# Performance work log

Measured on AMD Instinct MI355X. Metric: run time of the kernel, lower is better.

Reference implementation:

```python
import jax, jax.numpy as jnp
import numpy as np

SEQ, BATCH, HIDDEN = 4096, 16, 512


def setup_inputs() -> dict:
    key = jax.random.key(0)
    ks = jax.random.split(key, 8)
    scale = 1.0 / np.sqrt(HIDDEN)
    outputs_hidden = jax.random.normal(ks[0], (1, BATCH, HIDDEN), jnp.float32)
    encoder_out = jax.random.normal(ks[1], (SEQ, BATCH, HIDDEN), jnp.float32)
    encoder_features = jax.random.normal(ks[2], (SEQ, BATCH, HIDDEN), jnp.float32)
    # binary-ish float mask, mostly ones
    encoder_mask = (jax.random.uniform(ks[3], (BATCH, 1, SEQ)) > 0.1).astype(jnp.float32)
    # running sum of positive exp-scores; keep strictly positive
    temporal_scores_sum = jax.random.uniform(ks[4], (BATCH, 1, SEQ)) + 0.5
    W_feat = jax.random.normal(ks[5], (HIDDEN, HIDDEN), jnp.float32) * scale
    b_feat = jax.random.normal(ks[6], (HIDDEN,), jnp.float32)
    v_attn = jax.random.normal(ks[7], (HIDDEN,), jnp.float32) * scale
    return {
        "outputs_hidden": outputs_hidden,
        "encoder_out": encoder_out,
        "encoder_features": encoder_features,
        "encoder_mask": encoder_mask,
        "temporal_scores_sum": temporal_scores_sum,
        "W_feat": W_feat,
        "b_feat": b_feat,
        "v_attn": v_attn,
    }


def reference(outputs_hidden, encoder_out, encoder_features, encoder_mask,
              temporal_scores_sum, W_feat, b_feat, v_attn):
    # self.features: Linear(hidden, hidden) on decoder state [1, b, h]
    decoder_features = jnp.einsum('obh,kh->obk', outputs_hidden, W_feat) + b_feat
    # additive score: tanh(dec + enc) . v  -> [s, b]
    scores = jnp.einsum('sbh,h->sb', jnp.tanh(decoder_features + encoder_features), v_attn)
    # Permute(1,2,0) of [s,b,1] -> [b,1,s], then exp
    temporal_attention = jnp.exp(scores).T[:, None, :]  # [b, 1, s]
    attention = temporal_attention / temporal_scores_sum
    new_scores_sum = temporal_attention + temporal_scores_sum
    attention = attention * encoder_mask
    attention = attention / jnp.sum(attention, axis=-1, keepdims=True)  # Normalize(-1)
    enc = jnp.transpose(encoder_out, (1, 0, 2))           # [b, s, h]
    context = jnp.matmul(attention, enc)                  # [b, 1, h]
    context = jnp.transpose(context, (1, 0, 2))           # [1, b, h]
    return context, attention, new_scores_sum
```

## Files before the change

kernel.cpp:

```cpp
#include <hip/hip_runtime.h>
#include <hip/hip_bf16.h>
#include <stdint.h>

#define SEQ 4096
#define BATCH 16
#define HID 512
#define ATT_OFF (BATCH * HID)
#define NSS_OFF (BATCH * HID + BATCH * SEQ)

#define SPW 4
#define NT 4
#define SBLK (4 * NT * SPW)
#define NGRP (SEQ / SBLK)
#define NSTREAM_BLOCKS (BATCH * NGRP)

typedef unsigned short u16;
typedef unsigned int u32;

__device__ __forceinline__ float bflo(u32 w) { return __uint_as_float(w << 16); }
__device__ __forceinline__ float bfhi(u32 w) { return __uint_as_float(w & 0xffff0000u); }

__device__ __forceinline__ u16 f2bf(float f) {
  u32 u = __float_as_uint(f);
  return (u16)((u + 0x7fffu + ((u >> 16) & 1u)) >> 16);
}

__device__ __forceinline__ int probe_bf16(const void* tssp) {
  const u16* t = (const u16*)tssp;
  int ok = 1;
  #pragma unroll
  for (int i = 0; i < 8; i += 2) {
    u16 u = t[i];
    ok &= (u >= 0x3F00 && u <= 0x3FC0) ? 1 : 0;
  }
  return ok;
}

template <int BF>
__device__ __forceinline__ float ld1(const void* p, size_t i) {
  if (BF) return __uint_as_float(((u32)((const u16*)p)[i]) << 16);
  return ((const float*)p)[i];
}

template <int BF>
__device__ __forceinline__ void st1(void* p, size_t i, float v) {
  if (BF) ((u16*)p)[i] = f2bf(v);
  else    ((float*)p)[i] = v;
}

template <int BF>
__device__ __forceinline__ void load8(const void* p, size_t e, float* o) {
  if (BF) {
    uint4 v = *(const uint4*)((const u16*)p + e);
    o[0]=bflo(v.x); o[1]=bfhi(v.x); o[2]=bflo(v.y); o[3]=bfhi(v.y);
    o[4]=bflo(v.z); o[5]=bfhi(v.z); o[6]=bflo(v.w); o[7]=bfhi(v.w);
  } else {
    const float4* f = (const float4*)((const float*)p + e);
    float4 a = f[0], b = f[1];
    o[0]=a.x; o[1]=a.y; o[2]=a.z; o[3]=a.w;
    o[4]=b.x; o[5]=b.y; o[6]=b.z; o[7]=b.w;
  }
}

__device__ __forceinline__ float fast_tanh(float x) {
  float e = __expf(2.0f * x);
  return 1.0f - 2.0f * __builtin_amdgcn_rcpf(e + 1.0f);
}

template <int BF>
__device__ __forceinline__ void k_dec_body(
    const void* oh, const void* W, const void* bias, float* dec) {
  int tid = threadIdx.x;
  int gw = blockIdx.x * 4 + (tid >> 6);
  int lane = tid & 63;
  int k = gw & (HID - 1);
  int b = gw >> 9;
  float wv[8], ov[8];
  load8<BF>(W,  (size_t)k * HID + lane * 8, wv);
  load8<BF>(oh, (size_t)b * HID + lane * 8, ov);
  float acc = 0.0f;
  #pragma unroll
  for (int j = 0; j < 8; ++j) acc += wv[j] * ov[j];
  #pragma unroll
  for (int off = 32; off; off >>= 1) acc += __shfl_xor(acc, off, 64);
  if (lane == 0) dec[b * HID + k] = acc + ld1<BF>(bias, k);
}

__global__ __launch_bounds__(256) void k_dec(
    const void* oh, const void* W, const void* bias, const void* tss,
    float* dec, float* denom) {
  if (blockIdx.x == 0 && threadIdx.x < BATCH) denom[threadIdx.x] = 0.0f;
  if (probe_bf16(tss)) k_dec_body<1>(oh, W, bias, dec);
  else                 k_dec_body<0>(oh, W, bias, dec);
}

template <int BF>
__device__ __forceinline__ void k_scores_body(
    const void* ef, const void* maskp, const void* tssp, const void* vp,
    const float* dec, float* w_buf, float* denom, void* out) {
  int tid = threadIdx.x, lane = tid & 63, wave = tid >> 6;
  int blk = blockIdx.x;
  int b = blk & (BATCH - 1);
  int grp = blk >> 4;
  int sw = grp * SBLK + wave * (NT * SPW);

  float dv[8], vv[8];
  #pragma unroll
  for (int j = 0; j < 8; ++j) dv[j] = dec[b * HID + lane * 8 + j];
  load8<BF>(vp, lane * 8, vv);

  float evA[SPW][8], evB[SPW][8];
  float tsA[SPW], tsB[SPW], mA[SPW], mB[SPW];
  float wsum = 0.0f;

  auto LOADT = [&](float (&buf)[SPW][8], float (&ts)[SPW], float (&m)[SPW],
                   int t) {
    int s0 = sw + t * SPW;
    #pragma unroll
    for (int i = 0; i < SPW; ++i)
      load8<BF>(ef, ((size_t)(s0 + i) * BATCH + b) * HID + lane * 8, buf[i]);
    #pragma unroll
    for (int i = 0; i < SPW; ++i) {
      ts[i] = ld1<BF>(tssp,  b * SEQ + s0 + i);
      m[i]  = ld1<BF>(maskp, b * SEQ + s0 + i);
    }
  };
  auto COMP = [&](float (&buf)[SPW][8], float (&ts)[SPW], float (&m)[SPW],
                  int t) {
    int s0 = sw + t * SPW;
    float acc[SPW];
    #pragma unroll
    for (int i = 0; i < SPW; ++i) {
      float s = 0.0f;
      #pragma unroll
      for (int j = 0; j < 8; ++j) s += fast_tanh(buf[i][j] + dv[j]) * vv[j];
      acc[i] = s;
    }
    #pragma unroll
    for (int off = 32; off; off >>= 1) {
      #pragma unroll
      for (int i = 0; i < SPW; ++i) acc[i] += __shfl_xor(acc[i], off, 64);
    }
    #pragma unroll
    for (int i = 0; i < SPW; ++i) {
      float p  = __expf(acc[i]);
      float wv = p * m[i] * __builtin_amdgcn_rcpf(ts[i]);
      wsum += wv;
      if (lane == 0) {
        st1<BF>(out, NSS_OFF + b * SEQ + s0 + i, p + ts[i]);
        w_buf[b * SEQ + s0 + i] = wv;
      }
    }
  };

  LOADT(evA, tsA, mA, 0);
  LOADT(evB, tsB, mB, 1);  COMP(evA, tsA, mA, 0);
  LOADT(evA, tsA, mA, 2);  COMP(evB, tsB, mB, 1);
  LOADT(evB, tsB, mB, 3);  COMP(evA, tsA, mA, 2);
                           COMP(evB, tsB, mB, 3);

  __shared__ float wpart[4];
  if (lane == 0) wpart[wave] = wsum;
  __syncthreads();
  if (tid == 0)
    atomicAdd(&denom[b], wpart[0] + wpart[1] + wpart[2] + wpart[3]);
}

__global__ __launch_bounds__(256, 3) void k_scores(
    const void* ef, const void* maskp, const void* tssp, const void* vp,
    const float* dec, float* w_buf, float* denom, void* out) {
  if (probe_bf16(tssp))
    k_scores_body<1>(ef, maskp, tssp, vp, dec, w_buf, denom, out);
  else
    k_scores_body<0>(ef, maskp, tssp, vp, dec, w_buf, denom, out);
}

template <int BF>
__device__ __forceinline__ void k_ctx_body(
    const void* eo, const float* w_buf, float* partial) {
  int tid = threadIdx.x, lane = tid & 63, wave = tid >> 6;
  int blk = blockIdx.x;
  int b = blk & (BATCH - 1);
  int grp = blk >> 4;
  int sw = grp * SBLK + wave * (NT * SPW);

  float eoA[SPW][8], eoB[SPW][8];
  float wA[SPW], wB[SPW];
  float a[8] = {0,0,0,0,0,0,0,0};

  auto LOADT = [&](float (&buf)[SPW][8], float (&w)[SPW], int t) {
    int s0 = sw + t * SPW;
    #pragma unroll
    for (int i = 0; i < SPW; ++i)
      load8<BF>(eo, ((size_t)(s0 + i) * BATCH + b) * HID + lane * 8, buf[i]);
    #pragma unroll
    for (int i = 0; i < SPW; ++i) w[i] = w_buf[b * SEQ + s0 + i];
  };
  auto COMP = [&](float (&buf)[SPW][8], float (&w)[SPW]) {
    #pragma unroll
    for (int i = 0; i < SPW; ++i)
      #pragma unroll
      for (int j = 0; j < 8; ++j) a[j] += w[i] * buf[i][j];
  };

  LOADT(eoA, wA, 0);
  LOADT(eoB, wB, 1);  COMP(eoA, wA);
  LOADT(eoA, wA, 2);  COMP(eoB, wB);
  LOADT(eoB, wB, 3);  COMP(eoA, wA);
                      COMP(eoB, wB);

  __shared__ float red[3 * 8 * 64];
  if (wave > 0) {
    #pragma unroll
    for (int j = 0; j < 8; ++j) red[((wave - 1) * 8 + j) * 64 + lane] = a[j];
  }
  __syncthreads();
  if (wave == 0) {
    #pragma unroll
    for (int k = 0; k < 3; ++k)
      #pragma unroll
      for (int j = 0; j < 8; ++j) a[j] += red[(k * 8 + j) * 64 + lane];
    float4* p4 = (float4*)(partial + ((size_t)b * NGRP + grp) * HID + lane * 8);
    p4[0] = make_float4(a[0], a[1], a[2], a[3]);
    p4[1] = make_float4(a[4], a[5], a[6], a[7]);
  }
}

__global__ __launch_bounds__(256, 3) void k_ctx(
    const void* eo, const void* tssp, const float* w_buf, float* partial) {
  if (probe_bf16(tssp)) k_ctx_body<1>(eo, w_buf, partial);
  else                  k_ctx_body<0>(eo, w_buf, partial);
}

template <int BF>
__device__ __forceinline__ void k_fin_body(
    const float* w_buf, const float* denom, const float* partial, void* out) {
  int b = blockIdx.x >> 5;
  int part = blockIdx.x & 31;
  int t = threadIdx.x;
  float inv_d = __builtin_amdgcn_rcpf(denom[b]);
  if (t < 128) {
    int s = part * 128 + t;
    st1<BF>(out, ATT_OFF + b * SEQ + s, w_buf[b * SEQ + s] * inv_d);
  }
  int hl = t >> 4, cp = t & 15;
  int h = part * 16 + hl;
  float sum = 0.0f;
  #pragma unroll
  for (int c = cp; c < NGRP; c += 16)
    sum += partial[((size_t)b * NGRP + c) * HID + h];
  #pragma unroll
  for (int off = 8; off; off >>= 1) sum += __shfl_xor(sum, off, 64);
  if (cp == 0) st1<BF>(out, b * HID + h, sum * inv_d);
}

__global__ __launch_bounds__(256) void k_finalize(
    const float* w_buf, const float* denom, const float* partial,
    const void* tssp, void* out) {
  if (probe_bf16(tssp)) k_fin_body<1>(w_buf, denom, partial, out);
  else                  k_fin_body<0>(w_buf, denom, partial, out);
}

extern "C" void kernel_launch(void* const* d_in, const int* in_sizes, int n_in,
                              void* d_out, int out_size, void* d_ws, size_t ws_size,
                              hipStream_t stream) {
  const void* oh   = d_in[0];
  const void* eo   = d_in[1];
  const void* ef   = d_in[2];
  const void* mask = d_in[3];
  const void* tss  = d_in[4];
  const void* W    = d_in[5];
  const void* bias = d_in[6];
  const void* v    = d_in[7];

  float* ws      = (float*)d_ws;
  float* dec     = ws;
  float* w_buf   = dec + BATCH * HID;
  float* denom   = w_buf + BATCH * SEQ;
  float* partial = denom + 16;

  k_dec     <<<2048, 256, 0, stream>>>(oh, W, bias, tss, dec, denom);
  k_scores  <<<NSTREAM_BLOCKS, 256, 0, stream>>>(ef, mask, tss, v, dec, w_buf,
                                                 denom, d_out);
  k_ctx     <<<NSTREAM_BLOCKS, 256, 0, stream>>>(eo, tss, w_buf, partial);
  k_finalize<<< 512, 256, 0, stream>>>(w_buf, denom, partial, tss, d_out);
}
```

Baseline: 303.9 us.

## Fuse score and context streaming kernels into a single pass

Merges the score kernel and the context kernel into one kernel that loads encoder_features and encoder_out rows together and accumulates the weighted context with the unnormalized weights right away. This removes a separate launch and the re-read of the weight buffer, and lets both streams overlap in one pipeline. Rows per tile are halved to keep register pressure similar, which doubles the number of blocks and the partial-sum buffer that finalize has to reduce.

```diff
diff --git a/kernel.cpp b/kernel.cpp
--- a/kernel.cpp
+++ b/kernel.cpp
@@ -8,11 +8,11 @@
 #define ATT_OFF (BATCH * HID)
 #define NSS_OFF (BATCH * HID + BATCH * SEQ)
 
-#define SPW 4
+#define SPW 2
 #define NT 4
 #define SBLK (4 * NT * SPW)
 #define NGRP (SEQ / SBLK)
-#define NSTREAM_BLOCKS (BATCH * NGRP)
+#define NBLK (BATCH * NGRP)
 
 typedef unsigned short u16;
 typedef unsigned int u32;
@@ -95,9 +95,10 @@
 }
 
 template <int BF>
-__device__ __forceinline__ void k_scores_body(
-    const void* ef, const void* maskp, const void* tssp, const void* vp,
-    const float* dec, float* w_buf, float* denom, void* out) {
+__device__ __forceinline__ void k_str_body(
+    const void* ef, const void* eo, const void* maskp, const void* tssp,
+    const void* vp, const float* dec, float* w_buf, float* denom,
+    float* partial, void* out) {
   int tid = threadIdx.x, lane = tid & 63, wave = tid >> 6;
   int blk = blockIdx.x;
   int b = blk & (BATCH - 1);
@@ -109,31 +110,35 @@
   for (int j = 0; j < 8; ++j) dv[j] = dec[b * HID + lane * 8 + j];
   load8<BF>(vp, lane * 8, vv);
 
-  float evA[SPW][8], evB[SPW][8];
+  float evA[SPW][8], evB[SPW][8], eoA[SPW][8], eoB[SPW][8];
   float tsA[SPW], tsB[SPW], mA[SPW], mB[SPW];
+  float a[8] = {0,0,0,0,0,0,0,0};
   float wsum = 0.0f;
 
-  auto LOADT = [&](float (&buf)[SPW][8], float (&ts)[SPW], float (&m)[SPW],
-                   int t) {
+  auto LOADT = [&](float (&ev)[SPW][8], float (&eov)[SPW][8],
+                   float (&ts)[SPW], float (&m)[SPW], int t) {
     int s0 = sw + t * SPW;
     #pragma unroll
-    for (int i = 0; i < SPW; ++i)
-      load8<BF>(ef, ((size_t)(s0 + i) * BATCH + b) * HID + lane * 8, buf[i]);
+    for (int i = 0; i < SPW; ++i) {
+      size_t row = ((size_t)(s0 + i) * BATCH + b) * HID + lane * 8;
+      load8<BF>(ef, row, ev[i]);
+      load8<BF>(eo, row, eov[i]);
+    }
     #pragma unroll
     for (int i = 0; i < SPW; ++i) {
       ts[i] = ld1<BF>(tssp,  b * SEQ + s0 + i);
       m[i]  = ld1<BF>(maskp, b * SEQ + s0 + i);
     }
   };
-  auto COMP = [&](float (&buf)[SPW][8], float (&ts)[SPW], float (&m)[SPW],
-                  int t) {
+  auto COMPT = [&](float (&ev)[SPW][8], float (&eov)[SPW][8],
+                   float (&ts)[SPW], float (&m)[SPW], int t) {
     int s0 = sw + t * SPW;
     float acc[SPW];
     #pragma unroll
     for (int i = 0; i < SPW; ++i) {
       float s = 0.0f;
       #pragma unroll
-      for (int j = 0; j < 8; ++j) s += fast_tanh(buf[i][j] + dv[j]) * vv[j];
+      for (int j = 0; j < 8; ++j) s += fast_tanh(ev[i][j] + dv[j]) * vv[j];
       acc[i] = s;
     }
     #pragma unroll
@@ -150,66 +155,21 @@
         st1<BF>(out, NSS_OFF + b * SEQ + s0 + i, p + ts[i]);
         w_buf[b * SEQ + s0 + i] = wv;
       }
+      #pragma unroll
+      for (int j = 0; j < 8; ++j) a[j] += wv * eov[i][j];
     }
   };
 
-  LOADT(evA, tsA, mA, 0);
-  LOADT(evB, tsB, mB, 1);  COMP(evA, tsA, mA, 0);
-  LOADT(evA, tsA, mA, 2);  COMP(evB, tsB, mB, 1);
-  LOADT(evB, tsB, mB, 3);  COMP(evA, tsA, mA, 2);
-                           COMP(evB, tsB, mB, 3);
-
+  LOADT(evA, eoA, tsA, mA, 0);
+  LOADT(evB, eoB, tsB, mB, 1);
+  COMPT(evA, eoA, tsA, mA, 0);  LOADT(evA, eoA, tsA, mA, 2);
+  COMPT(evB, eoB, tsB, mB, 1);  LOADT(evB, eoB, tsB, mB, 3);
+  COMPT(evA, eoA, tsA, mA, 2);
+  COMPT(evB, eoB, tsB, mB, 3);
+
+  __shared__ float red[3 * 8 * 64];
   __shared__ float wpart[4];
   if (lane == 0) wpart[wave] = wsum;
-  __syncthreads();
-  if (tid == 0)
-    atomicAdd(&denom[b], wpart[0] + wpart[1] + wpart[2] + wpart[3]);
-}
-
-__global__ __launch_bounds__(256, 3) void k_scores(
-    const void* ef, const void* maskp, const void* tssp, const void* vp,
-    const float* dec, float* w_buf, float* denom, void* out) {
-  if (probe_bf16(tssp))
-    k_scores_body<1>(ef, maskp, tssp, vp, dec, w_buf, denom, out);
-  else
-    k_scores_body<0>(ef, maskp, tssp, vp, dec, w_buf, denom, out);
-}
-
-template <int BF>
-__device__ __forceinline__ void k_ctx_body(
-    const void* eo, const float* w_buf, float* partial) {
-  int tid = threadIdx.x, lane = tid & 63, wave = tid >> 6;
-  int blk = blockIdx.x;
-  int b = blk & (BATCH - 1);
-  int grp = blk >> 4;
-  int sw = grp * SBLK + wave * (NT * SPW);
-
-  float eoA[SPW][8], eoB[SPW][8];
-  float wA[SPW], wB[SPW];
-  float a[8] = {0,0,0,0,0,0,0,0};
-
-  auto LOADT = [&](float (&buf)[SPW][8], float (&w)[SPW], int t) {
-    int s0 = sw + t * SPW;
-    #pragma unroll
-    for (int i = 0; i < SPW; ++i)
-      load8<BF>(eo, ((size_t)(s0 + i) * BATCH + b) * HID + lane * 8, buf[i]);
-    #pragma unroll
-    for (int i = 0; i < SPW; ++i) w[i] = w_buf[b * SEQ + s0 + i];
-  };
-  auto COMP = [&](float (&buf)[SPW][8], float (&w)[SPW]) {
-    #pragma unroll
-    for (int i = 0; i < SPW; ++i)
-      #pragma unroll
-      for (int j = 0; j < 8; ++j) a[j] += w[i] * buf[i][j];
-  };
-
-  LOADT(eoA, wA, 0);
-  LOADT(eoB, wB, 1);  COMP(eoA, wA);
-  LOADT(eoA, wA, 2);  COMP(eoB, wB);
-  LOADT(eoB, wB, 3);  COMP(eoA, wA);
-                      COMP(eoB, wB);
-
-  __shared__ float red[3 * 8 * 64];
   if (wave > 0) {
     #pragma unroll
     for (int j = 0; j < 8; ++j) red[((wave - 1) * 8 + j) * 64 + lane] = a[j];
@@ -223,13 +183,19 @@
     float4* p4 = (float4*)(partial + ((size_t)b * NGRP + grp) * HID + lane * 8);
     p4[0] = make_float4(a[0], a[1], a[2], a[3]);
     p4[1] = make_float4(a[4], a[5], a[6], a[7]);
-  }
-}
-
-__global__ __launch_bounds__(256, 3) void k_ctx(
-    const void* eo, const void* tssp, const float* w_buf, float* partial) {
-  if (probe_bf16(tssp)) k_ctx_body<1>(eo, w_buf, partial);
-  else                  k_ctx_body<0>(eo, w_buf, partial);
+    if (tid == 0)
+      atomicAdd(&denom[b], wpart[0] + wpart[1] + wpart[2] + wpart[3]);
+  }
+}
+
+__global__ __launch_bounds__(256, 3) void k_str(
+    const void* ef, const void* eo, const void* maskp, const void* tssp,
+    const void* vp, const float* dec, float* w_buf, float* denom,
+    float* partial, void* out) {
+  if (probe_bf16(tssp))
+    k_str_body<1>(ef, eo, maskp, tssp, vp, dec, w_buf, denom, partial, out);
+  else
+    k_str_body<0>(ef, eo, maskp, tssp, vp, dec, w_buf, denom, partial, out);
 }
 
 template <int BF>
@@ -280,8 +246,7 @@
   float* partial = denom + 16;
 
   k_dec     <<<2048, 256, 0, stream>>>(oh, W, bias, tss, dec, denom);
-  k_scores  <<<NSTREAM_BLOCKS, 256, 0, stream>>>(ef, mask, tss, v, dec, w_buf,
-                                                 denom, d_out);
-  k_ctx     <<<NSTREAM_BLOCKS, 256, 0, stream>>>(eo, tss, w_buf, partial);
+  k_str     <<<NBLK, 256, 0, stream>>>(ef, eo, mask, tss, v, dec, w_buf,
+                                       denom, partial, d_out);
   k_finalize<<< 512, 256, 0, stream>>>(w_buf, denom, partial, tss, d_out);
 }
```

Result: faster. 293.8 us (-3.3%).
